# Performance work log

Measured on AMD Instinct MI355X. Metric: run time of the kernel, lower is better.

Reference implementation:

```python
import math
import jax, jax.numpy as jnp
import numpy as np

EMBED_DIM = 1024
NUM_HEADS = 16
HEAD_DIM = EMBED_DIM // NUM_HEADS


def setup_inputs() -> dict:
    key = jax.random.key(0)
    k1, k2, k3, k4 = jax.random.split(key, 4)
    B, S = 4, 2048
    x = jax.random.normal(k1, (B, S, EMBED_DIM), dtype=jnp.float32)
    mask = jnp.ones((B, S), dtype=jnp.int32)  # key-padding mask, 1 = keep
    # nn.Linear(embed_dim, 3*embed_dim, bias=False): weight [3E, E]
    w_qkv = jax.random.normal(k2, (3 * EMBED_DIM, EMBED_DIM), dtype=jnp.float32) / math.sqrt(EMBED_DIM)
    # nn.Linear(embed_dim, embed_dim): weight [E, E], bias [E]
    w_out = jax.random.normal(k3, (EMBED_DIM, EMBED_DIM), dtype=jnp.float32) / math.sqrt(EMBED_DIM)
    b_out = jax.random.normal(k4, (EMBED_DIM,), dtype=jnp.float32) * 0.01
    return {"x": x, "w_qkv": w_qkv, "w_out": w_out, "b_out": b_out, "mask": mask}


def _attention(x, w_qkv, w_out, b_out, mask):
    B, S, E = x.shape
    qkv = jnp.einsum("bse,fe->bsf", x, w_qkv)  # [B,S,3E]
    q, k, v = jnp.split(qkv, 3, axis=-1)
    def heads(t):  # [B,S,E] -> [B,H,S,D]
        return t.reshape(B, S, NUM_HEADS, HEAD_DIM).transpose(0, 2, 1, 3)
    q, k, v = heads(q), heads(k), heads(v)
    scores = jnp.einsum("bhqd,bhkd->bhqk", q, k) / math.sqrt(HEAD_DIM)
    keep = (mask != 0)[:, None, None, :]  # [B,1,1,S]
    scores = jnp.where(keep, scores, jnp.float32(-1e9))
    probs = jax.nn.softmax(scores, axis=-1)
    # dropout p=0.0 -> identity (eval semantics)
    out = jnp.einsum("bhqk,bhkd->bhqd", probs, v)
    out = out.transpose(0, 2, 1, 3).reshape(B, S, E)
    return jnp.einsum("bse,fe->bsf", out, w_out) + b_out


def reference(x, w_qkv, w_out, b_out, mask):
    return _attention(x, w_qkv, w_out, b_out, mask)
```

## Files before the change

kernel.cpp:

```cpp
#include <hip/hip_runtime.h>

#define EMB 1024
#define NH 16
#define HD 64
#define SEQ 2048
#define BB 4

typedef __attribute__((ext_vector_type(8))) short bf8;
typedef __attribute__((ext_vector_type(4))) short bf4;
typedef __attribute__((ext_vector_type(4))) float f4;

#define MFMA16(a, b, c) __builtin_amdgcn_mfma_f32_16x16x32_bf16((a), (b), (c), 0, 0, 0)

#if defined(__has_builtin)
#if __has_builtin(__builtin_amdgcn_mfma_f32_16x16x16_bf16_1k)
#define HAVE_MFMA16X16 1
#endif
#if __has_builtin(__builtin_amdgcn_exp2f)
#define EXP2F __builtin_amdgcn_exp2f
#endif
#if __has_builtin(__builtin_amdgcn_cvt_pk_bf16_f32)
#define HAVE_PK_BF16 1
#endif
#if __has_builtin(__builtin_amdgcn_perm)
#define HAVE_PERM 1
#endif
#endif
#ifndef EXP2F
#define EXP2F exp2f
#endif

__device__ inline f4 pv_mfma(bf4 a, bf4 b, f4 c) {
#ifdef HAVE_MFMA16X16
  return __builtin_amdgcn_mfma_f32_16x16x16_bf16_1k(a, b, c, 0, 0, 0);
#else
  bf8 av, bv;
  *(bf4*)&av = a;  ((int*)&av)[2] = 0; ((int*)&av)[3] = 0;
  *(bf4*)&bv = b;  ((int*)&bv)[2] = 0; ((int*)&bv)[3] = 0;
  return __builtin_amdgcn_mfma_f32_16x16x32_bf16(av, bv, c, 0, 0, 0);
#endif
}

#define GLL16(g, l)                                                     \
  __builtin_amdgcn_global_load_lds(                                     \
      (__attribute__((address_space(1))) void*)(g),                     \
      (__attribute__((address_space(3))) void*)(l), 16, 0, 0)

__device__ inline unsigned short f2bf(float f) {
  union { float f; unsigned u; } v; v.f = f;
  unsigned u = v.u;
  u += 0x7fffu + ((u >> 16) & 1u);
  return (unsigned short)(u >> 16);
}

__device__ inline unsigned pkbf(float a, float b) {
#ifdef HAVE_PK_BF16
  typedef __attribute__((ext_vector_type(2))) __bf16 bf16x2;
  union { bf16x2 v; unsigned u; } c;
  c.v = __builtin_amdgcn_cvt_pk_bf16_f32(a, b);
  return c.u;
#elif defined(HAVE_PERM)
  union { float f; unsigned u; } ua, ub; ua.f = a; ub.f = b;
  return __builtin_amdgcn_perm(ub.u + 0x8000u, ua.u + 0x8000u, 0x07060302u);
#else
  union { float f; unsigned u; } ua, ub; ua.f = a; ub.f = b;
  return ((ua.u + 0x8000u) >> 16) | ((ub.u + 0x8000u) & 0xFFFF0000u);
#endif
}

#define SCALE_LOG2E 0.1803368801111244f

__global__ void cvt_all(const float* __restrict__ x, const float* __restrict__ wq,
                        const float* __restrict__ wo, unsigned short* __restrict__ out) {
  int i = blockIdx.x * blockDim.x + threadIdx.x;
  float4 f;
  if (i < 2097152)      f = ((const float4*)x)[i];
  else if (i < 2883584) f = ((const float4*)wq)[i - 2097152];
  else                  f = ((const float4*)wo)[i - 2883584];
  ushort4 o;
  o.x = f2bf(f.x); o.y = f2bf(f.y); o.z = f2bf(f.z); o.w = f2bf(f.w);
  ((ushort4*)out)[i] = o;
}

template <bool OUTF32>
__global__ __launch_bounds__(256, 3) void gemm_bt(
    const unsigned short* __restrict__ A, const unsigned short* __restrict__ B,
    void* __restrict__ Cout, const float* __restrict__ bias,
    unsigned short* __restrict__ vtb,
    int M, int N, int K, int ldC, int nsplit) {
  __shared__ unsigned short la[2][128 * 32];
  __shared__ unsigned short lb[2][128 * 32];

  const int t = threadIdx.x;
  const int lane = t & 63;
  const int w = t >> 6;
  const int quad = lane >> 4;
  const int lcol = lane & 15;

  const int nbx = gridDim.x;
  const int flat = blockIdx.y * nbx + blockIdx.x;
  const int nper = (nbx * gridDim.y) >> 3;
  const int sw = (flat & 7) * nper + (flat >> 3);
  const int m0 = (sw / nbx) * 128;
  const int n0 = (sw % nbx) * 128;

  const int wm = (w & 1) * 64;
  const int wn = (w >> 1) * 64;

  f4 acc[4][4];
#pragma unroll
  for (int i = 0; i < 4; i++)
#pragma unroll
    for (int j = 0; j < 4; j++) acc[i][j] = (f4){0.f, 0.f, 0.f, 0.f};

  const int srow = t >> 2;
  const int scol = (t & 3) * 8;
  const unsigned short* gA = A + (size_t)(m0 + srow) * K + scol;
  const unsigned short* gB = B + (size_t)(n0 + srow) * K + scol;

  GLL16(gA, la[0] + t * 8);
  GLL16(gA + (size_t)64 * K, la[0] + 64 * 32 + t * 8);
  GLL16(gB, lb[0] + t * 8);
  GLL16(gB + (size_t)64 * K, lb[0] + 64 * 32 + t * 8);

  const int nk = K >> 5;
  for (int it = 0; it < nk; ++it) {
    const int cur = it & 1;
    __syncthreads();

    if (it + 1 < nk) {
      const int nxt = cur ^ 1;
      const int kt = (it + 1) << 5;
      GLL16(gA + kt, la[nxt] + t * 8);
      GLL16(gA + kt + (size_t)64 * K, la[nxt] + 64 * 32 + t * 8);
      GLL16(gB + kt, lb[nxt] + t * 8);
      GLL16(gB + kt + (size_t)64 * K, lb[nxt] + 64 * 32 + t * 8);
    }

    bf8 af[4], bfr[4];
#pragma unroll
    for (int i = 0; i < 4; i++) {
      af[i]  = *(const bf8*)&la[cur][(wm + i * 16 + lcol) * 32 + quad * 8];
      bfr[i] = *(const bf8*)&lb[cur][(wn + i * 16 + lcol) * 32 + quad * 8];
    }
#pragma unroll
    for (int i = 0; i < 4; i++)
#pragma unroll
      for (int j = 0; j < 4; j++)
        acc[i][j] = MFMA16(af[i], bfr[j], acc[i][j]);
  }

  if (!OUTF32 && n0 >= nsplit) {
#pragma unroll
    for (int i = 0; i < 4; i++) {
#pragma unroll
      for (int j = 0; j < 4; j++) {
        int f = n0 + wn + j * 16 + lcol - nsplit;
        int mg = m0 + wm + i * 16 + quad * 4;
        int bb = mg >> 11, ss = mg & 2047;
        ushort4 pk;
        pk.x = f2bf(acc[i][j][0]); pk.y = f2bf(acc[i][j][1]);
        pk.z = f2bf(acc[i][j][2]); pk.w = f2bf(acc[i][j][3]);
        *(ushort4*)&vtb[((size_t)(bb * 1024 + f)) * 2048 + ss] = pk;
      }
    }
  } else {
#pragma unroll
    for (int i = 0; i < 4; i++) {
#pragma unroll
      for (int j = 0; j < 4; j++) {
        int n = n0 + wn + j * 16 + lcol;
        const float scl = (!OUTF32 && n >= 1024) ? SCALE_LOG2E : 1.f;
#pragma unroll
        for (int r = 0; r < 4; r++) {
          int m = m0 + wm + i * 16 + quad * 4 + r;
          if (OUTF32) {
            float v = acc[i][j][r] + (bias ? bias[n] : 0.f);
            ((float*)Cout)[(size_t)m * ldC + n] = v;
          } else {
            ((unsigned short*)Cout)[(size_t)m * ldC + n] = f2bf(acc[i][j][r] * scl);
          }
        }
      }
    }
  }
}

#define BKEEP (-16.0f)
#define BDROP (-1e30f)

__global__ __launch_bounds__(512, 4) void attn_kernel(
    const unsigned short* __restrict__ qk, const unsigned short* __restrict__ vtg,
    const int* __restrict__ mask, unsigned short* __restrict__ outb) {
  __shared__ unsigned short kv[2 * 16384];
  __shared__ __align__(16) float bt[2][128];

  const int t = threadIdx.x;
  const int lane = t & 63;
  const int w = t >> 6;
  const int quad = lane >> 4;
  const int lcol = lane & 15;
  const int lx = lcol & 7;

  const int id = blockIdx.x + (blockIdx.y << 4) + (blockIdx.z << 8);
  const int g  = (id & 7) + ((id >> 7) << 3);
  const int q0 = ((id >> 3) & 15) * 128;
  const int h = g & 15;
  const int b = g >> 4;

  const unsigned short* qbase = qk + (size_t)(b * SEQ) * 2048 + h * HD;
  const unsigned short* kbase = qbase + 1024;
  const unsigned short* vbase = vtg + (size_t)((b * 16 + h) * 64) * SEQ;

  const int qrow = q0 + w * 16 + lcol;
  const bf8 qf0 = *(const bf8*)(qbase + (size_t)qrow * 2048 + quad * 8);
  const bf8 qf1 = *(const bf8*)(qbase + (size_t)qrow * 2048 + 32 + quad * 8);

  f4 o[4];
#pragma unroll
  for (int db = 0; db < 4; db++) o[db] = (f4){0.f, 0.f, 0.f, 0.f};
  float lsum = 0.f;

  const int sr = t >> 3;
  const int sc = ((t & 7) ^ (sr & 7)) * 8;
  const unsigned short* gk = kbase + (size_t)sr * 2048 + sc;
  const int vd = t >> 4;
  const int vc8 = ((t & 15) ^ (vd & 7)) * 8;
  const unsigned short* gv = vbase + (size_t)vd * SEQ + vc8;

  const int NT = SEQ / 128;

  GLL16(gk, kv + t * 8);
  GLL16(gk + (size_t)64 * 2048, kv + 4096 + t * 8);
  GLL16(gv, kv + 8192 + t * 8);
  GLL16(gv + (size_t)32 * SEQ, kv + 12288 + t * 8);
  if (t < 128) bt[0][t] = mask[b * SEQ + t] ? BKEEP : BDROP;
  int pmv = (t < 128) ? mask[b * SEQ + 128 + t] : 0;

  for (int it = 0; it < NT; ++it) {
    const int cur = (it & 1) * 16384;
    __syncthreads();

    if (it + 1 < NT) {
      const int nxt = ((it + 1) & 1) * 16384;
      const size_t k1 = (size_t)(it + 1) * 128;
      GLL16(gk + k1 * 2048, kv + nxt + t * 8);
      GLL16(gk + (k1 + 64) * 2048, kv + nxt + 4096 + t * 8);
      GLL16(gv + k1, kv + nxt + 8192 + t * 8);
      GLL16(gv + (size_t)32 * SEQ + k1, kv + nxt + 12288 + t * 8);
      if (t < 128) bt[(it + 1) & 1][t] = pmv ? BKEEP : BDROP;
      int kn = (it + 2 < NT) ? (it + 2) * 128 : 0;
      pmv = (t < 128) ? mask[b * SEQ + kn + t] : 0;
    }

    const unsigned short* kcur = kv + cur;
    const unsigned short* vcur = kv + cur + 8192;
    const float* bcur = bt[it & 1];

#pragma unroll
    for (int hh = 0; hh < 2; hh++) {
      f4 sT[4];
      __builtin_amdgcn_s_setprio(1);
#pragma unroll
      for (int kb = 0; kb < 4; kb++) {
        const unsigned short* krow = kcur + (hh * 64 + kb * 16 + lcol) * 64;
        bf8 kf0 = *(const bf8*)&krow[(quad ^ lx) * 8];
        bf8 kf1 = *(const bf8*)&krow[((4 + quad) ^ lx) * 8];
        f4 a = *(const f4*)&bcur[hh * 64 + kb * 16 + quad * 4];
        a = MFMA16(kf0, qf0, a);
        a = MFMA16(kf1, qf1, a);
        sT[kb] = a;
      }
      __builtin_amdgcn_s_setprio(0);

      bf4 pfrag[4];
#pragma unroll
      for (int kb = 0; kb < 4; kb++) {
        float p0 = EXP2F(sT[kb][0]);
        float p1 = EXP2F(sT[kb][1]);
        float p2 = EXP2F(sT[kb][2]);
        float p3 = EXP2F(sT[kb][3]);
        lsum += (p0 + p1) + (p2 + p3);
        union { unsigned u[2]; bf4 s; } cv;
        cv.u[0] = pkbf(p0, p1);
        cv.u[1] = pkbf(p2, p3);
        pfrag[kb] = cv.s;
      }

      __builtin_amdgcn_s_setprio(1);
#pragma unroll
      for (int db = 0; db < 4; db++) {
        const unsigned short* vrow = vcur + (db * 16 + lcol) * 128;
#pragma unroll
        for (int kb = 0; kb < 4; kb++) {
          int c = ((hh * 4 + kb) << 1) | (quad >> 1);
          bf4 vf = *(const bf4*)&vrow[(c ^ lx) * 8 + (quad & 1) * 4];
          o[db] = pv_mfma(vf, pfrag[kb], o[db]);
        }
      }
      __builtin_amdgcn_s_setprio(0);
    }
  }

  lsum += __shfl_xor(lsum, 16);
  lsum += __shfl_xor(lsum, 32);
  float inv = 1.f / lsum;
#pragma unroll
  for (int db = 0; db < 4; db++) {
    ushort4 pk;
    pk.x = f2bf(o[db][0] * inv);
    pk.y = f2bf(o[db][1] * inv);
    pk.z = f2bf(o[db][2] * inv);
    pk.w = f2bf(o[db][3] * inv);
    *(ushort4*)&outb[(size_t)(b * SEQ + q0 + w * 16 + lcol) * EMB + h * HD +
                     db * 16 + quad * 4] = pk;
  }
}

extern "C" void kernel_launch(void* const* d_in, const int* in_sizes, int n_in,
                              void* d_out, int out_size, void* d_ws, size_t ws_size,
                              hipStream_t stream) {
  const float* x     = (const float*)d_in[0];
  const float* w_qkv = (const float*)d_in[1];
  const float* w_out = (const float*)d_in[2];
  const float* b_out = (const float*)d_in[3];
  const int*   mask  = (const int*)d_in[4];

  char* ws = (char*)d_ws;
  unsigned short* xb    = (unsigned short*)(ws + 0);
  unsigned short* wqkvb = (unsigned short*)(ws + 16777216);
  unsigned short* woutb = (unsigned short*)(ws + 23068672);
  unsigned short* qkb   = (unsigned short*)(ws + 25165824);
  unsigned short* attnb = (unsigned short*)(ws + 58720256);
  unsigned short* vtb   = (unsigned short*)(ws + 75497472);

  cvt_all<<<12288, 256, 0, stream>>>(x, w_qkv, w_out, (unsigned short*)ws);

  gemm_bt<false><<<dim3(24, 64), 256, 0, stream>>>(
      xb, wqkvb, (void*)qkb, nullptr, vtb, 8192, 3072, 1024, 2048, 2048);

  attn_kernel<<<dim3(16, 16, 4), 512, 0, stream>>>(qkb, vtb, mask, attnb);

  gemm_bt<true><<<dim3(8, 64), 256, 0, stream>>>(
      attnb, woutb, d_out, b_out, nullptr, 8192, 1024, 1024, 1024, 1 << 30);
}
```

Before: 305.8 us.

## Add 256x256-tile 8-wave QKV GEMM with interleaved staging and setprio

Replaces the generic 128-tile QKV projection GEMM with a dedicated kernel that uses 256x256 output tiles, 512 threads, a K-step of 64 and double-buffered LDS. Global-to-LDS staging for the next tile is interleaved between four MFMA quadrants, with explicit vmcnt waits and barriers, and MFMA bursts are raised in priority. Block indices are swizzled for L2 locality. The aim is more data reuse per tile and better overlap of loads with MFMA, at the cost of higher register and LDS pressure (128KB of LDS, 2 blocks per CU) and scalar bf16 stores in the Q/K epilogue.

```diff
diff --git a/kernel.cpp b/kernel.cpp
--- a/kernel.cpp
+++ b/kernel.cpp
@@ -82,6 +82,156 @@
   ((ushort4*)out)[i] = o;
 }
 
+#define PSYNC(VMSTR)                                          \
+  do {                                                        \
+    asm volatile("s_waitcnt " VMSTR ::: "memory");            \
+    __builtin_amdgcn_s_barrier();                             \
+    asm volatile("" ::: "memory");                            \
+  } while (0)
+#define PSYNC_NOVM()                                          \
+  do {                                                        \
+    asm volatile("" ::: "memory");                            \
+    __builtin_amdgcn_s_barrier();                             \
+    asm volatile("" ::: "memory");                            \
+  } while (0)
+
+__global__ __launch_bounds__(512, 2) void gemm_qkv8(
+    const unsigned short* __restrict__ A, const unsigned short* __restrict__ B,
+    unsigned short* __restrict__ qkb, unsigned short* __restrict__ vtb) {
+  __shared__ unsigned short lA[2][256 * 64];
+  __shared__ unsigned short lB[2][256 * 64];
+  const int K = 1024;
+
+  const int t = threadIdx.x;
+  const int lane = t & 63;
+  const int w = t >> 6;
+  const int quad = lane >> 4;
+  const int lcol = lane & 15;
+  const int lx7 = lcol & 15 & 7;
+
+  const int flat = blockIdx.x;
+  const int sw = (flat & 7) * 48 + (flat >> 3);
+  const int m0 = (sw / 12) * 256;
+  const int n0 = (sw % 12) * 256;
+
+  const int wm = (w & 1) * 128;
+  const int wn = (w >> 1) * 64;
+
+  f4 acc[8][4];
+#pragma unroll
+  for (int i = 0; i < 8; i++)
+#pragma unroll
+    for (int j = 0; j < 4; j++) acc[i][j] = (f4){0.f, 0.f, 0.f, 0.f};
+
+  const int srow = t >> 3;
+  const int schunk = (t & 7) ^ (srow & 7);
+  const unsigned short* gA = A + (size_t)(m0 + srow) * K + schunk * 8;
+  const int bcol1 = srow + (srow & 32);
+  const unsigned short* gB0 = B + (size_t)n0 * K + schunk * 8;
+
+#define STAGE_A(bufi, rb, kt1)                                               \
+  do {                                                                       \
+    GLL16(gA + (size_t)(rb) * K + (kt1), &lA[bufi][(rb) * 64 + t * 8]);      \
+    GLL16(gA + (size_t)((rb) + 128) * K + (kt1),                             \
+          &lA[bufi][((rb) + 128) * 64 + t * 8]);                             \
+  } while (0)
+#define STAGE_B(bufi, cb, kt1)                                               \
+  do {                                                                       \
+    GLL16(gB0 + (size_t)((cb) + bcol1) * K + (kt1),                          \
+          &lB[bufi][((cb) + bcol1) * 64 + (t & 7) * 8]);                     \
+    GLL16(gB0 + (size_t)((cb) + bcol1 + 128) * K + (kt1),                    \
+          &lB[bufi][((cb) + bcol1 + 128) * 64 + (t & 7) * 8]);               \
+  } while (0)
+
+  bf8 af[4][2], bfr[2][2];
+#define LOAD_AF(cb, mq)                                                      \
+  _Pragma("unroll") for (int i = 0; i < 4; i++) _Pragma("unroll")            \
+      for (int kk = 0; kk < 2; kk++)                                         \
+          af[i][kk] = *(const bf8*)&lA[cb][(wm + (mq)*64 + i * 16 + lcol) *  \
+                                              64 +                          \
+                                          (((kk << 2) | quad) ^ lx7) * 8]
+#define LOAD_BF(cb, nq)                                                      \
+  _Pragma("unroll") for (int j = 0; j < 2; j++) _Pragma("unroll")            \
+      for (int kk = 0; kk < 2; kk++)                                         \
+          bfr[j][kk] = *(const bf8*)&lB[cb][(wn + (nq)*32 + j * 16 + lcol) * \
+                                               64 +                         \
+                                           (((kk << 2) | quad) ^ lx7) * 8]
+#define MFMA_Q(mq, nq)                                                       \
+  do {                                                                       \
+    __builtin_amdgcn_s_setprio(1);                                           \
+    _Pragma("unroll") for (int i = 0; i < 4; i++) _Pragma("unroll")          \
+        for (int j = 0; j < 2; j++) _Pragma("unroll")                        \
+            for (int kk = 0; kk < 2; kk++)                                   \
+                acc[(mq)*4 + i][(nq)*2 + j] =                                \
+                    MFMA16(af[i][kk], bfr[j][kk], acc[(mq)*4 + i][(nq)*2 + j]); \
+    __builtin_amdgcn_s_setprio(0);                                           \
+  } while (0)
+
+  STAGE_A(0, 0, 0);
+  STAGE_B(0, 0, 0);
+  STAGE_A(0, 64, 0);
+  STAGE_B(0, 32, 0);
+
+  const int nk = K / 64;
+  for (int kt = 0; kt < nk; ++kt) {
+    const int cur = kt & 1;
+    const int nxt = cur ^ 1;
+    const int k1 = (kt + 1) * 64;
+    const bool st = (kt + 1 < nk);
+
+    PSYNC("vmcnt(4)");
+    LOAD_AF(cur, 0);
+    LOAD_BF(cur, 0);
+    if (st) STAGE_A(nxt, 0, k1);
+    MFMA_Q(0, 0);
+
+    if (st) PSYNC("vmcnt(4)"); else PSYNC("vmcnt(2)");
+    LOAD_AF(cur, 1);
+    if (st) STAGE_B(nxt, 0, k1);
+    MFMA_Q(1, 0);
+
+    if (st) PSYNC("vmcnt(4)"); else PSYNC("vmcnt(0)");
+    LOAD_BF(cur, 1);
+    if (st) STAGE_A(nxt, 64, k1);
+    MFMA_Q(1, 1);
+
+    PSYNC_NOVM();
+    LOAD_AF(cur, 0);
+    if (st) STAGE_B(nxt, 32, k1);
+    MFMA_Q(0, 1);
+  }
+
+  if (n0 >= 2048) {
+#pragma unroll
+    for (int MF = 0; MF < 8; MF++) {
+#pragma unroll
+      for (int NF = 0; NF < 4; NF++) {
+        int f = n0 - 2048 + wn + NF * 16 + lcol;
+        int mg = m0 + wm + MF * 16 + quad * 4;
+        int bb = mg >> 11, ss = mg & 2047;
+        ushort4 pk;
+        pk.x = f2bf(acc[MF][NF][0]); pk.y = f2bf(acc[MF][NF][1]);
+        pk.z = f2bf(acc[MF][NF][2]); pk.w = f2bf(acc[MF][NF][3]);
+        *(ushort4*)&vtb[((size_t)(bb * 1024 + f)) * 2048 + ss] = pk;
+      }
+    }
+  } else {
+    const float scl = (n0 >= 1024) ? SCALE_LOG2E : 1.f;
+#pragma unroll
+    for (int MF = 0; MF < 8; MF++) {
+#pragma unroll
+      for (int NF = 0; NF < 4; NF++) {
+        int n = n0 + wn + NF * 16 + lcol;
+#pragma unroll
+        for (int r = 0; r < 4; r++) {
+          int m = m0 + wm + MF * 16 + quad * 4 + r;
+          qkb[(size_t)m * 2048 + n] = f2bf(acc[MF][NF][r] * scl);
+        }
+      }
+    }
+  }
+}
+
 template <bool OUTF32>
 __global__ __launch_bounds__(256, 3) void gemm_bt(
     const unsigned short* __restrict__ A, const unsigned short* __restrict__ B,
@@ -336,8 +486,7 @@
 
   cvt_all<<<12288, 256, 0, stream>>>(x, w_qkv, w_out, (unsigned short*)ws);
 
-  gemm_bt<false><<<dim3(24, 64), 256, 0, stream>>>(
-      xb, wqkvb, (void*)qkb, nullptr, vtb, 8192, 3072, 1024, 2048, 2048);
+  gemm_qkv8<<<384, 512, 0, stream>>>(xb, wqkvb, qkb, vtb);
 
   attn_kernel<<<dim3(16, 16, 4), 512, 0, stream>>>(qkb, vtb, mask, attnb);
 
```

New measurement: 317.0 us. 3.7% more time.
